# Performance work log

Measured on AMD Instinct MI355X. Metric: run time of the kernel, lower is better.

Reference implementation:

```python
import jax, jax.numpy as jnp
import numpy as np

N, E, H, L, IN, OUT = 50000, 800000, 64, 14, 128, 112
MSG_EPS = 1e-7   # GENConv message epsilon
LN_EPS = 1e-5    # torch.nn.LayerNorm default eps


def setup_inputs() -> dict:
    key = jax.random.key(0)
    ks = jax.random.split(key, 8)
    s = 0.05
    x = jax.random.normal(ks[0], (N, IN), jnp.float32)
    edge_index = jax.random.randint(ks[1], (2, E), 0, N, dtype=jnp.int64)
    enc_W = jax.random.normal(ks[2], (IN, H), jnp.float32) * s
    enc_b = jnp.zeros((H,), jnp.float32)
    ln_g = jnp.ones((L, H), jnp.float32)
    ln_b = jnp.zeros((L, H), jnp.float32)
    mlp_W = jax.random.normal(ks[3], (L, H, H), jnp.float32) * s
    mlp_b = jnp.zeros((L, H), jnp.float32)
    pred_W = jax.random.normal(ks[4], (H, OUT), jnp.float32) * s
    pred_b = jnp.zeros((OUT,), jnp.float32)
    return dict(x=x, edge_index=edge_index, enc_W=enc_W, enc_b=enc_b,
                ln_g=ln_g, ln_b=ln_b, mlp_W=mlp_W, mlp_b=mlp_b,
                pred_W=pred_W, pred_b=pred_b)


def _layernorm(h, g, b):
    mu = jnp.mean(h, axis=-1, keepdims=True)
    var = jnp.mean(jnp.square(h - mu), axis=-1, keepdims=True)  # biased, as torch
    return (h - mu) * jax.lax.rsqrt(var + LN_EPS) * g + b


def _genconv(h, src, dst, W, b):
    # GENConv: msg = relu(x_src) + eps; softmax aggregation (t=1) over dst; out = Linear(x + agg)
    msg = jax.nn.relu(h[src]) + MSG_EPS                    # [E, H]
    mmax = jax.ops.segment_max(msg, dst, num_segments=N)   # [N, H]
    mmax = jnp.where(jnp.isfinite(mmax), mmax, 0.0)         # empty segments
    ex = jnp.exp(msg - mmax[dst])                           # [E, H]
    denom = jax.ops.segment_sum(ex, dst, num_segments=N)    # [N, H]
    num = jax.ops.segment_sum(msg * ex, dst, num_segments=N)
    agg = num / jnp.maximum(denom, 1e-16)                   # 0 for isolated nodes
    return (h + agg) @ W + b


def reference(x, edge_index, enc_W, enc_b, ln_g, ln_b, mlp_W, mlp_b, pred_W, pred_b):
    src, dst = edge_index[0], edge_index[1]
    h = x @ enc_W + enc_b                       # node feature encoder
    h = _genconv(h, src, dst, mlp_W[0], mlp_b[0])  # first GCN (no pre-norm in res+)

    def body(h, params):
        g, bl, W, b = params
        h2 = jax.nn.relu(_layernorm(h, g, bl))  # dropout is identity (eval)
        h = _genconv(h2, src, dst, W, b) + h    # residual
        return h, None

    h, _ = jax.lax.scan(body, h, (ln_g[:L - 1], ln_b[:L - 1], mlp_W[1:], mlp_b[1:]))
    return h @ pred_W + pred_b
```

## Files before the change

### kernel.cpp

```cpp
#include <hip/hip_runtime.h>
#include <hip/hip_bf16.h>

#define NN 50000
#define EE 800000
#define HD 64
#define LL 14
#define IND 128
#define OUTD 112
#define LN2 0.69314718056f

typedef __attribute__((ext_vector_type(8))) short short8;
typedef __attribute__((ext_vector_type(4))) float float4_;
typedef __attribute__((ext_vector_type(4))) unsigned short ushort4_;

__device__ __forceinline__ short bf16_hi(float x) {
    return (short)(__float_as_uint(x) >> 16);
}
__device__ __forceinline__ float bf16_f(short s) {
    return __uint_as_float(((unsigned)(unsigned short)s) << 16);
}
__device__ __forceinline__ float us2f(unsigned short u) {
    return __uint_as_float(((unsigned)u) << 16);
}
__device__ __forceinline__ unsigned short f2b_rne(float x) {
    unsigned u = __float_as_uint(x);
    u += 0x7fffu + ((u >> 16) & 1u);
    return (unsigned short)(u >> 16);
}

__device__ __forceinline__ void split8(const float* p, short8& hi, short8& lo) {
    float4_ a = *(const float4_*)p;
    float4_ b = *(const float4_*)(p + 4);
    float v[8] = {a[0], a[1], a[2], a[3], b[0], b[1], b[2], b[3]};
    #pragma unroll
    for (int j = 0; j < 8; ++j) {
        short h = bf16_hi(v[j]);
        hi[j] = h;
        lo[j] = bf16_hi(v[j] - bf16_f(h));
    }
}

__device__ __forceinline__ void load_b(const float* __restrict__ W, int ldw,
                                       int colbase, int krow, short8& hi, short8& lo) {
    #pragma unroll
    for (int j = 0; j < 8; ++j) {
        float wv = W[(krow + j) * ldw + colbase];
        short h = bf16_hi(wv);
        hi[j] = h;
        lo[j] = bf16_hi(wv - bf16_f(h));
    }
}

__device__ __forceinline__ float4_ mm3(short8 ah, short8 al, short8 bh, short8 bl,
                                       float4_ acc) {
    acc = __builtin_amdgcn_mfma_f32_16x16x32_bf16(ah, bh, acc, 0, 0, 0);
    acc = __builtin_amdgcn_mfma_f32_16x16x32_bf16(al, bh, acc, 0, 0, 0);
    acc = __builtin_amdgcn_mfma_f32_16x16x32_bf16(ah, bl, acc, 0, 0, 0);
    return acc;
}


__global__ void k_hist(const int* __restrict__ ei, int* __restrict__ cnt,
                       int* __restrict__ rank) {
    int e = blockIdx.x * blockDim.x + threadIdx.x;
    if (e < EE) rank[e] = atomicAdd(&cnt[ei[EE + e]], 1);
}

__global__ __launch_bounds__(1024) void k_scan1(const int* __restrict__ deg,
                                                int* __restrict__ excl,
                                                int* __restrict__ bsum) {
    __shared__ int ws[16];
    int tid = threadIdx.x, lane = tid & 63, w = tid >> 6;
    int gid = blockIdx.x * 1024 + tid;
    int v = (gid < NN) ? deg[gid] : 0;
    int x = v;
    #pragma unroll
    for (int d = 1; d < 64; d <<= 1) {
        int y = __shfl_up(x, d);
        if (lane >= d) x += y;
    }
    if (lane == 63) ws[w] = x;
    __syncthreads();
    if (tid == 0) {
        int acc = 0;
        for (int i = 0; i < 16; i++) { int t = ws[i]; ws[i] = acc; acc += t; }
        bsum[blockIdx.x] = acc;
    }
    __syncthreads();
    if (gid < NN) excl[gid] = x - v + ws[w];
}

__global__ void k_scan2(const int* __restrict__ bsum, int* __restrict__ boff, int nb) {
    if (threadIdx.x == 0) {
        int acc = 0;
        for (int i = 0; i < nb; i++) { boff[i] = acc; acc += bsum[i]; }
    }
}

__global__ __launch_bounds__(1024) void k_scan3(int* __restrict__ rp,
                                                const int* __restrict__ boff) {
    int gid = blockIdx.x * 1024 + threadIdx.x;
    if (gid < NN) rp[gid] += boff[blockIdx.x];
    if (gid == 0) rp[NN] = EE;
}

__global__ void k_scatter(const int* __restrict__ ei, const int* __restrict__ rp,
                          const int* __restrict__ rank, int* __restrict__ csrc) {
    int e = blockIdx.x * blockDim.x + threadIdx.x;
    if (e < EE) {
        int d = ei[EE + e];
        csrc[rp[d] + rank[e]] = ei[e];
    }
}


__global__ __launch_bounds__(256) void k_enc(const float* __restrict__ x,
                                             const float* __restrict__ W,
                                             const float* __restrict__ b,
                                             float* __restrict__ h,
                                             unsigned short* __restrict__ P0) {
    __shared__ float X[16 * 132];
    int tid = threadIdx.x, lane = tid & 63, w = tid >> 6;
    int nb = blockIdx.x * 16;
    int nq = lane >> 4, nr = lane & 15;
    int colbase = w * 16 + nr;

    {
        const float* src = x + (size_t)nb * IND + tid * 8;
        float4_ a = *(const float4_*)src;
        float4_ c = *(const float4_*)(src + 4);
        int m = tid >> 4, k8 = 8 * (tid & 15);
        *(float4_*)&X[m * 132 + k8] = a;
        *(float4_*)&X[m * 132 + k8 + 4] = c;
    }
    __syncthreads();

    float4_ acc = {};
    #pragma unroll
    for (int t = 0; t < 4; ++t) {
        short8 ah, al, bh, bl;
        split8(&X[nr * 132 + t * 32 + nq * 8], ah, al);
        load_b(W, HD, colbase, t * 32 + nq * 8, bh, bl);
        acc = mm3(ah, al, bh, bl, acc);
    }

    float bias = b[colbase];
    #pragma unroll
    for (int r = 0; r < 4; ++r) {
        int node = nb + nq * 4 + r;
        float y = acc[r] + bias;
        h[node * HD + colbase] = y;
        float msg = fminf(fmaxf(y, 0.f) + 1e-7f, 50.f);
        P0[node * HD + colbase] = f2b_rne(__expf(msg));
    }
}


__global__ __launch_bounds__(256) void k_layer(const unsigned short* __restrict__ Pin,
                                               const float* __restrict__ selfh,
                                               const float* __restrict__ hres,
                                               float* __restrict__ hout,
                                               unsigned short* __restrict__ Pout,
                                               const int* __restrict__ rp,
                                               const int* __restrict__ csrc,
                                               const float* __restrict__ W,
                                               const float* __restrict__ b,
                                               const float* __restrict__ gnext,
                                               const float* __restrict__ bnext) {
    __shared__ float T[16 * 68];
    int tid = threadIdx.x, lane = tid & 63, w = tid >> 6;
    int nb = blockIdx.x * 16;
    int nq = lane >> 4, nr = lane & 15;
    int colbase = w * 16 + nr;

    short8 Bhi[2], Blo[2];
    #pragma unroll
    for (int t = 0; t < 2; ++t)
        load_b(W, HD, colbase, t * 32 + nq * 8, Bhi[t], Blo[t]);

    int g = lane >> 4;
    int ci = lane & 15;
    #pragma unroll 1
    for (int i = 0; i < 4; ++i) {
        int node = nb + w * 4 + i;
        int beg = rp[node], end = rp[node + 1], deg = end - beg;
        float s0 = 0.f, s1 = 0.f, s2 = 0.f, s3 = 0.f;
        float n0 = 0.f, n1 = 0.f, n2 = 0.f, n3 = 0.f;
        for (int chunk = 0; chunk < deg; chunk += 64) {
            int cnt = min(64, deg - chunk);
            int myidx = 0;
            if (chunk + lane < deg) myidx = csrc[beg + chunk + lane];
            int nb4 = (cnt + 3) >> 2;
            #pragma unroll 2
            for (int k = 0; k < nb4; ++k) {
                int src = __shfl(myidx, k * 4 + g);
                const unsigned* pp = (const unsigned*)(Pin + ((size_t)src << 6)) + ci * 2;
                unsigned d0 = pp[0], d1 = pp[1];
                if (k * 4 + g >= cnt) { d0 = 0u; d1 = 0u; }
                float p0 = __uint_as_float(d0 << 16);
                float p1 = __uint_as_float(d0 & 0xffff0000u);
                float p2 = __uint_as_float(d1 << 16);
                float p3 = __uint_as_float(d1 & 0xffff0000u);
                s0 += p0; s1 += p1; s2 += p2; s3 += p3;
                n0 = fmaf(p0, __log2f(fmaxf(p0, 1e-20f)), n0);
                n1 = fmaf(p1, __log2f(fmaxf(p1, 1e-20f)), n1);
                n2 = fmaf(p2, __log2f(fmaxf(p2, 1e-20f)), n2);
                n3 = fmaf(p3, __log2f(fmaxf(p3, 1e-20f)), n3);
            }
        }
        #pragma unroll
        for (int d = 16; d < 64; d <<= 1) {
            s0 += __shfl_xor(s0, d); s1 += __shfl_xor(s1, d);
            s2 += __shfl_xor(s2, d); s3 += __shfl_xor(s3, d);
            n0 += __shfl_xor(n0, d); n1 += __shfl_xor(n1, d);
            n2 += __shfl_xor(n2, d); n3 += __shfl_xor(n3, d);
        }
        if (g == 0) {
            float a0 = LN2 * n0 / fmaxf(s0, 1e-16f);
            float a1 = LN2 * n1 / fmaxf(s1, 1e-16f);
            float a2 = LN2 * n2 / fmaxf(s2, 1e-16f);
            float a3 = LN2 * n3 / fmaxf(s3, 1e-16f);
            float4_ xv;
            if (selfh) {
                float4_ sf = *(const float4_*)&selfh[(size_t)node * HD + ci * 4];
                xv[0] = sf[0] + a0; xv[1] = sf[1] + a1;
                xv[2] = sf[2] + a2; xv[3] = sf[3] + a3;
            } else {
                const unsigned* pp = (const unsigned*)(Pin + ((size_t)node << 6)) + ci * 2;
                unsigned d0 = pp[0], d1 = pp[1];
                xv[0] = LN2 * __log2f(__uint_as_float(d0 << 16)) - 1e-7f + a0;
                xv[1] = LN2 * __log2f(__uint_as_float(d0 & 0xffff0000u)) - 1e-7f + a1;
                xv[2] = LN2 * __log2f(__uint_as_float(d1 << 16)) - 1e-7f + a2;
                xv[3] = LN2 * __log2f(__uint_as_float(d1 & 0xffff0000u)) - 1e-7f + a3;
            }
            *(float4_*)&T[(w * 4 + i) * 68 + ci * 4] = xv;
        }
    }
    __syncthreads();

    short8 Ahi[2], Alo[2];
    #pragma unroll
    for (int t = 0; t < 2; ++t)
        split8(&T[nr * 68 + t * 32 + nq * 8], Ahi[t], Alo[t]);
    __syncthreads();

    float4_ acc = {};
    #pragma unroll
    for (int t = 0; t < 2; ++t)
        acc = mm3(Ahi[t], Alo[t], Bhi[t], Blo[t], acc);

    float bias = b[colbase];
    #pragma unroll
    for (int r = 0; r < 4; ++r) {
        int m = nq * 4 + r;
        int node = nb + m;
        float v = acc[r] + bias;
        if (hres) v += hres[node * HD + colbase];
        hout[node * HD + colbase] = v;
        T[m * 68 + colbase] = v;
    }
    if (!Pout) return;
    __syncthreads();

    int m = tid >> 4, c4 = (tid & 15) * 4;
    float4_ vv = *(const float4_*)&T[m * 68 + c4];
    float ps_ = (vv[0] + vv[1]) + (vv[2] + vv[3]);
    float pq_ = (vv[0] * vv[0] + vv[1] * vv[1]) + (vv[2] * vv[2] + vv[3] * vv[3]);
    #pragma unroll
    for (int d = 8; d; d >>= 1) {
        ps_ += __shfl_xor(ps_, d);
        pq_ += __shfl_xor(pq_, d);
    }
    float mu = ps_ * (1.f / 64.f);
    float var = pq_ * (1.f / 64.f) - mu * mu;
    float inv = rsqrtf(fmaxf(var, 0.f) + 1e-5f);
    float4_ g4 = *(const float4_*)&gnext[c4];
    float4_ b4 = *(const float4_*)&bnext[c4];
    ushort4_ po;
    #pragma unroll
    for (int j = 0; j < 4; ++j) {
        float y = fmaxf((vv[j] - mu) * inv * g4[j] + b4[j], 0.f);
        float msg = fminf(y + 1e-7f, 50.f);
        po[j] = f2b_rne(__expf(msg));
    }
    *(ushort4_*)&Pout[(nb + m) * HD + c4] = po;
}


__global__ __launch_bounds__(256) void k_pred(const float* __restrict__ h,
                                              const float* __restrict__ W,
                                              const float* __restrict__ b,
                                              float* __restrict__ out) {
    __shared__ float T[16 * 68];
    int tid = threadIdx.x, lane = tid & 63, w = tid >> 6;
    int nb = blockIdx.x * 16;
    int nq = lane >> 4, nr = lane & 15;

    {
        const float* src = h + (size_t)nb * HD + tid * 4;
        float4_ a = *(const float4_*)src;
        int m = tid >> 4, k4 = 4 * (tid & 15);
        *(float4_*)&T[m * 68 + k4] = a;
    }
    __syncthreads();

    short8 Ahi[2], Alo[2];
    #pragma unroll
    for (int t = 0; t < 2; ++t)
        split8(&T[nr * 68 + t * 32 + nq * 8], Ahi[t], Alo[t]);

    for (int tt = w; tt < 7; tt += 4) {
        int colbase = tt * 16 + nr;
        float4_ acc = {};
        #pragma unroll
        for (int t = 0; t < 2; ++t) {
            short8 bh, bl;
            load_b(W, OUTD, colbase, t * 32 + nq * 8, bh, bl);
            acc = mm3(Ahi[t], Alo[t], bh, bl, acc);
        }
        float bias = b[colbase];
        #pragma unroll
        for (int r = 0; r < 4; ++r) {
            int node = nb + nq * 4 + r;
            out[node * OUTD + colbase] = acc[r] + bias;
        }
    }
}


extern "C" void kernel_launch(void* const* d_in, const int* in_sizes, int n_in,
                              void* d_out, int out_size, void* d_ws, size_t ws_size,
                              hipStream_t stream) {
    const float* x    = (const float*)d_in[0];
    const int*   ei   = (const int*)d_in[1];
    const float* encW = (const float*)d_in[2];
    const float* encb = (const float*)d_in[3];
    const float* lng  = (const float*)d_in[4];
    const float* lnb  = (const float*)d_in[5];
    const float* mlpW = (const float*)d_in[6];
    const float* mlpb = (const float*)d_in[7];
    const float* pW   = (const float*)d_in[8];
    const float* pb   = (const float*)d_in[9];
    float* out = (float*)d_out;

    float* hA  = (float*)d_ws;
    float* hB  = hA + (size_t)NN * HD;
    unsigned short* PA = (unsigned short*)(hB + (size_t)NN * HD);
    unsigned short* PB = PA + (size_t)NN * HD;
    int* rp   = (int*)(PB + (size_t)NN * HD);
    int* cnt  = rp + (NN + 1);
    int* csrc = cnt + NN;
    int* rank = csrc + EE;
    int* bsum = rank + EE;
    int* boff = bsum + 64;

    hipMemsetAsync(cnt, 0, NN * sizeof(int), stream);
    k_hist<<<(EE + 255) / 256, 256, 0, stream>>>(ei, cnt, rank);
    const int NB = (NN + 1023) / 1024;
    k_scan1<<<NB, 1024, 0, stream>>>(cnt, rp, bsum);
    k_scan2<<<1, 64, 0, stream>>>(bsum, boff, NB);
    k_scan3<<<NB, 1024, 0, stream>>>(rp, boff);
    k_scatter<<<(EE + 255) / 256, 256, 0, stream>>>(ei, rp, rank, csrc);

    k_enc<<<NN / 16, 256, 0, stream>>>(x, encW, encb, hA, PA);

    k_layer<<<NN / 16, 256, 0, stream>>>(PA, hA, nullptr, hB, PB, rp, csrc,
                                         mlpW, mlpb, lng, lnb);

    float* hres = hB;
    float* hdst = hA;
    unsigned short* pc = PB;
    unsigned short* pn = PA;
    for (int l = 1; l < LL; ++l) {
        bool last = (l == LL - 1);
        k_layer<<<NN / 16, 256, 0, stream>>>(pc, nullptr, hres, hdst,
                                             last ? nullptr : pn,
                                             rp, csrc,
                                             mlpW + (size_t)l * HD * HD,
                                             mlpb + (size_t)l * HD,
                                             last ? nullptr : lng + (size_t)l * HD,
                                             last ? nullptr : lnb + (size_t)l * HD);
        float* t = hres; hres = hdst; hdst = t;
        unsigned short* u = pc; pc = pn; pn = u;
    }

    k_pred<<<NN / 16, 256, 0, stream>>>(hres, pW, pb, out);
}
```

Baseline: 736.2 us.

## Encode exp messages as bf16 codes with shared-memory p·log p lookup table, interleave four nodes

Messages are now stored as small integer codes (bf16 bits of exp(msg) minus an offset), and each block builds a shared-memory table of p and p·ln p for all codes. The per-edge log2 evaluations are replaced by LDS lookups. The four nodes per wave are also gathered in one interleaved loop up to the max degree, so four independent row loads are in flight at once. The cost is a per-block table build of about 1.5K entries with a sync, higher register pressure, and wasted lanes when node degrees differ.

```diff
diff --git a/kernel.cpp b/kernel.cpp
--- a/kernel.cpp
+++ b/kernel.cpp
@@ -8,8 +8,10 @@
 #define IND 128
 #define OUTD 112
 #define LN2 0.69314718056f
+#define LUTN 1537
 
 typedef __attribute__((ext_vector_type(8))) short short8;
+typedef __attribute__((ext_vector_type(2))) float float2_;
 typedef __attribute__((ext_vector_type(4))) float float4_;
 typedef __attribute__((ext_vector_type(4))) unsigned short ushort4_;
 
@@ -18,14 +20,15 @@
 }
 __device__ __forceinline__ float bf16_f(short s) {
     return __uint_as_float(((unsigned)(unsigned short)s) << 16);
-}
-__device__ __forceinline__ float us2f(unsigned short u) {
-    return __uint_as_float(((unsigned)u) << 16);
 }
 __device__ __forceinline__ unsigned short f2b_rne(float x) {
     unsigned u = __float_as_uint(x);
     u += 0x7fffu + ((u >> 16) & 1u);
     return (unsigned short)(u >> 16);
+}
+__device__ __forceinline__ unsigned short msg2code(float msg) {
+    int c = (int)f2b_rne(__expf(msg)) - 16255;
+    return (unsigned short)min(c, 1536);
 }
 
 __device__ __forceinline__ void split8(const float* p, short8& hi, short8& lo) {
@@ -118,7 +121,7 @@
                                              const float* __restrict__ W,
                                              const float* __restrict__ b,
                                              float* __restrict__ h,
-                                             unsigned short* __restrict__ P0) {
+                                             unsigned short* __restrict__ C0) {
     __shared__ float X[16 * 132];
     int tid = threadIdx.x, lane = tid & 63, w = tid >> 6;
     int nb = blockIdx.x * 16;
@@ -151,16 +154,16 @@
         float y = acc[r] + bias;
         h[node * HD + colbase] = y;
         float msg = fminf(fmaxf(y, 0.f) + 1e-7f, 50.f);
-        P0[node * HD + colbase] = f2b_rne(__expf(msg));
-    }
-}
-
-
-__global__ __launch_bounds__(256) void k_layer(const unsigned short* __restrict__ Pin,
+        C0[node * HD + colbase] = msg2code(msg);
+    }
+}
+
+
+__global__ __launch_bounds__(256) void k_layer(const unsigned short* __restrict__ Cin,
                                                const float* __restrict__ selfh,
                                                const float* __restrict__ hres,
                                                float* __restrict__ hout,
-                                               unsigned short* __restrict__ Pout,
+                                               unsigned short* __restrict__ Cout,
                                                const int* __restrict__ rp,
                                                const int* __restrict__ csrc,
                                                const float* __restrict__ W,
@@ -168,46 +171,79 @@
                                                const float* __restrict__ gnext,
                                                const float* __restrict__ bnext) {
     __shared__ float T[16 * 68];
+    __shared__ float L2lut[2 * 1540];
     int tid = threadIdx.x, lane = tid & 63, w = tid >> 6;
     int nb = blockIdx.x * 16;
     int nq = lane >> 4, nr = lane & 15;
     int colbase = w * 16 + nr;
 
+    for (int c = tid; c < LUTN; c += 256) {
+        float p = 0.f, q = 0.f;
+        if (c > 0) {
+            p = __uint_as_float((unsigned)(16255 + c) << 16);
+            q = p * (LN2 * __log2f(p));
+        }
+        L2lut[2 * c] = p;
+        L2lut[2 * c + 1] = q;
+    }
+
     short8 Bhi[2], Blo[2];
     #pragma unroll
     for (int t = 0; t < 2; ++t)
         load_b(W, HD, colbase, t * 32 + nq * 8, Bhi[t], Blo[t]);
+    __syncthreads();
 
     int g = lane >> 4;
     int ci = lane & 15;
-    #pragma unroll 1
+    int node0 = nb + w * 4;
+    int r0 = rp[node0], r1 = rp[node0 + 1], r2 = rp[node0 + 2],
+        r3 = rp[node0 + 3], r4 = rp[node0 + 4];
+    int beg[4] = {r0, r1, r2, r3};
+    int deg[4] = {r1 - r0, r2 - r1, r3 - r2, r4 - r3};
+    int maxdeg = max(max(deg[0], deg[1]), max(deg[2], deg[3]));
+
+    float S[4][4] = {{0.f}}, Nq[4][4] = {{0.f}};
+    for (int chunk = 0; chunk < maxdeg; chunk += 64) {
+        int myidx[4];
+        #pragma unroll
+        for (int i = 0; i < 4; ++i) {
+            myidx[i] = -1;
+            if (chunk + lane < deg[i]) myidx[i] = csrc[beg[i] + chunk + lane];
+        }
+        int cmax = min(64, maxdeg - chunk);
+        int nb4 = (cmax + 3) >> 2;
+        for (int k = 0; k < nb4; ++k) {
+            unsigned d0[4], d1[4];
+            #pragma unroll
+            for (int i = 0; i < 4; ++i) {
+                int src = __shfl(myidx[i], k * 4 + g);
+                const unsigned* pp =
+                    (const unsigned*)(Cin + ((size_t)max(src, 0) << 6)) + ci * 2;
+                unsigned a0 = pp[0], a1 = pp[1];
+                bool act = src >= 0;
+                d0[i] = act ? a0 : 0u;
+                d1[i] = act ? a1 : 0u;
+            }
+            #pragma unroll
+            for (int i = 0; i < 4; ++i) {
+                unsigned c0 = d0[i] & 0xffffu, c1 = d0[i] >> 16;
+                unsigned c2 = d1[i] & 0xffffu, c3 = d1[i] >> 16;
+                float2_ pq0 = *(const float2_*)&L2lut[c0 * 2];
+                float2_ pq1 = *(const float2_*)&L2lut[c1 * 2];
+                float2_ pq2 = *(const float2_*)&L2lut[c2 * 2];
+                float2_ pq3 = *(const float2_*)&L2lut[c3 * 2];
+                S[i][0] += pq0[0]; Nq[i][0] += pq0[1];
+                S[i][1] += pq1[0]; Nq[i][1] += pq1[1];
+                S[i][2] += pq2[0]; Nq[i][2] += pq2[1];
+                S[i][3] += pq3[0]; Nq[i][3] += pq3[1];
+            }
+        }
+    }
+
+    #pragma unroll
     for (int i = 0; i < 4; ++i) {
-        int node = nb + w * 4 + i;
-        int beg = rp[node], end = rp[node + 1], deg = end - beg;
-        float s0 = 0.f, s1 = 0.f, s2 = 0.f, s3 = 0.f;
-        float n0 = 0.f, n1 = 0.f, n2 = 0.f, n3 = 0.f;
-        for (int chunk = 0; chunk < deg; chunk += 64) {
-            int cnt = min(64, deg - chunk);
-            int myidx = 0;
-            if (chunk + lane < deg) myidx = csrc[beg + chunk + lane];
-            int nb4 = (cnt + 3) >> 2;
-            #pragma unroll 2
-            for (int k = 0; k < nb4; ++k) {
-                int src = __shfl(myidx, k * 4 + g);
-                const unsigned* pp = (const unsigned*)(Pin + ((size_t)src << 6)) + ci * 2;
-                unsigned d0 = pp[0], d1 = pp[1];
-                if (k * 4 + g >= cnt) { d0 = 0u; d1 = 0u; }
-                float p0 = __uint_as_float(d0 << 16);
-                float p1 = __uint_as_float(d0 & 0xffff0000u);
-                float p2 = __uint_as_float(d1 << 16);
-                float p3 = __uint_as_float(d1 & 0xffff0000u);
-                s0 += p0; s1 += p1; s2 += p2; s3 += p3;
-                n0 = fmaf(p0, __log2f(fmaxf(p0, 1e-20f)), n0);
-                n1 = fmaf(p1, __log2f(fmaxf(p1, 1e-20f)), n1);
-                n2 = fmaf(p2, __log2f(fmaxf(p2, 1e-20f)), n2);
-                n3 = fmaf(p3, __log2f(fmaxf(p3, 1e-20f)), n3);
-            }
-        }
+        float s0 = S[i][0], s1 = S[i][1], s2 = S[i][2], s3 = S[i][3];
+        float n0 = Nq[i][0], n1 = Nq[i][1], n2 = Nq[i][2], n3 = Nq[i][3];
         #pragma unroll
         for (int d = 16; d < 64; d <<= 1) {
             s0 += __shfl_xor(s0, d); s1 += __shfl_xor(s1, d);
@@ -216,22 +252,27 @@
             n2 += __shfl_xor(n2, d); n3 += __shfl_xor(n3, d);
         }
         if (g == 0) {
-            float a0 = LN2 * n0 / fmaxf(s0, 1e-16f);
-            float a1 = LN2 * n1 / fmaxf(s1, 1e-16f);
-            float a2 = LN2 * n2 / fmaxf(s2, 1e-16f);
-            float a3 = LN2 * n3 / fmaxf(s3, 1e-16f);
+            int node = node0 + i;
+            float a0 = n0 / fmaxf(s0, 1e-16f);
+            float a1 = n1 / fmaxf(s1, 1e-16f);
+            float a2 = n2 / fmaxf(s2, 1e-16f);
+            float a3 = n3 / fmaxf(s3, 1e-16f);
             float4_ xv;
             if (selfh) {
                 float4_ sf = *(const float4_*)&selfh[(size_t)node * HD + ci * 4];
                 xv[0] = sf[0] + a0; xv[1] = sf[1] + a1;
                 xv[2] = sf[2] + a2; xv[3] = sf[3] + a3;
             } else {
-                const unsigned* pp = (const unsigned*)(Pin + ((size_t)node << 6)) + ci * 2;
-                unsigned d0 = pp[0], d1 = pp[1];
-                xv[0] = LN2 * __log2f(__uint_as_float(d0 << 16)) - 1e-7f + a0;
-                xv[1] = LN2 * __log2f(__uint_as_float(d0 & 0xffff0000u)) - 1e-7f + a1;
-                xv[2] = LN2 * __log2f(__uint_as_float(d1 << 16)) - 1e-7f + a2;
-                xv[3] = LN2 * __log2f(__uint_as_float(d1 & 0xffff0000u)) - 1e-7f + a3;
+                const unsigned* pp = (const unsigned*)(Cin + ((size_t)node << 6)) + ci * 2;
+                unsigned e0 = pp[0], e1 = pp[1];
+                float2_ q0 = *(const float2_*)&L2lut[(e0 & 0xffffu) * 2];
+                float2_ q1 = *(const float2_*)&L2lut[(e0 >> 16) * 2];
+                float2_ q2 = *(const float2_*)&L2lut[(e1 & 0xffffu) * 2];
+                float2_ q3 = *(const float2_*)&L2lut[(e1 >> 16) * 2];
+                xv[0] = __fdividef(q0[1], q0[0]) - 1e-7f + a0;
+                xv[1] = __fdividef(q1[1], q1[0]) - 1e-7f + a1;
+                xv[2] = __fdividef(q2[1], q2[0]) - 1e-7f + a2;
+                xv[3] = __fdividef(q3[1], q3[0]) - 1e-7f + a3;
             }
             *(float4_*)&T[(w * 4 + i) * 68 + ci * 4] = xv;
         }
@@ -259,7 +300,7 @@
         hout[node * HD + colbase] = v;
         T[m * 68 + colbase] = v;
     }
-    if (!Pout) return;
+    if (!Cout) return;
     __syncthreads();
 
     int m = tid >> 4, c4 = (tid & 15) * 4;
@@ -281,9 +322,9 @@
     for (int j = 0; j < 4; ++j) {
         float y = fmaxf((vv[j] - mu) * inv * g4[j] + b4[j], 0.f);
         float msg = fminf(y + 1e-7f, 50.f);
-        po[j] = f2b_rne(__expf(msg));
-    }
-    *(ushort4_*)&Pout[(nb + m) * HD + c4] = po;
+        po[j] = msg2code(msg);
+    }
+    *(ushort4_*)&Cout[(nb + m) * HD + c4] = po;
 }
 
 
@@ -345,9 +386,9 @@
 
     float* hA  = (float*)d_ws;
     float* hB  = hA + (size_t)NN * HD;
-    unsigned short* PA = (unsigned short*)(hB + (size_t)NN * HD);
-    unsigned short* PB = PA + (size_t)NN * HD;
-    int* rp   = (int*)(PB + (size_t)NN * HD);
+    unsigned short* CA = (unsigned short*)(hB + (size_t)NN * HD);
+    unsigned short* CB = CA + (size_t)NN * HD;
+    int* rp   = (int*)(CB + (size_t)NN * HD);
     int* cnt  = rp + (NN + 1);
     int* csrc = cnt + NN;
     int* rank = csrc + EE;
@@ -362,26 +403,26 @@
     k_scan3<<<NB, 1024, 0, stream>>>(rp, boff);
     k_scatter<<<(EE + 255) / 256, 256, 0, stream>>>(ei, rp, rank, csrc);
 
-    k_enc<<<NN / 16, 256, 0, stream>>>(x, encW, encb, hA, PA);
-
-    k_layer<<<NN / 16, 256, 0, stream>>>(PA, hA, nullptr, hB, PB, rp, csrc,
+    k_enc<<<NN / 16, 256, 0, stream>>>(x, encW, encb, hA, CA);
+
+    k_layer<<<NN / 16, 256, 0, stream>>>(CA, hA, nullptr, hB, CB, rp, csrc,
                                          mlpW, mlpb, lng, lnb);
 
     float* hres = hB;
     float* hdst = hA;
-    unsigned short* pc = PB;
-    unsigned short* pn = PA;
+    unsigned short* cc = CB;
+    unsigned short* cn = CA;
     for (int l = 1; l < LL; ++l) {
         bool last = (l == LL - 1);
-        k_layer<<<NN / 16, 256, 0, stream>>>(pc, nullptr, hres, hdst,
-                                             last ? nullptr : pn,
+        k_layer<<<NN / 16, 256, 0, stream>>>(cc, nullptr, hres, hdst,
+                                             last ? nullptr : cn,
                                              rp, csrc,
                                              mlpW + (size_t)l * HD * HD,
                                              mlpb + (size_t)l * HD,
                                              last ? nullptr : lng + (size_t)l * HD,
                                              last ? nullptr : lnb + (size_t)l * HD);
         float* t = hres; hres = hdst; hdst = t;
-        unsigned short* u = pc; pc = pn; pn = u;
+        unsigned short* u = cc; cc = cn; cn = u;
     }
 
     k_pred<<<NN / 16, 256, 0, stream>>>(hres, pW, pb, out);
```

Measured after the change: 895.4 us. 21.6% more time.

## Pad CSR rows to multiples of four with a zero sentinel node

Applied to the files above, without the earlier changes.

Each node's CSR row is padded to a multiple of four edges, and the padding slots point to an extra all-zero feature row (index NN) added to both bf16 feature buffers. The aggregation loop then reads edge indices straight from memory per lane group, with no 64-wide chunking, shuffle broadcast or tail masking. This removes per-iteration shuffles and bounds checks from the hot gather loop. In exchange the edge array grows by up to 3N padding entries that each cost a real gather, and two small setup kernels are added. Zero padding rows contribute nothing because p*log2(max(p,eps)) is zero when p is zero.

```diff
diff --git a/kernel.cpp b/kernel.cpp
--- a/kernel.cpp
+++ b/kernel.cpp
@@ -19,9 +19,6 @@
 __device__ __forceinline__ float bf16_f(short s) {
     return __uint_as_float(((unsigned)(unsigned short)s) << 16);
 }
-__device__ __forceinline__ float us2f(unsigned short u) {
-    return __uint_as_float(((unsigned)u) << 16);
-}
 __device__ __forceinline__ unsigned short f2b_rne(float x) {
     unsigned u = __float_as_uint(x);
     u += 0x7fffu + ((u >> 16) & 1u);
@@ -72,7 +69,7 @@
     __shared__ int ws[16];
     int tid = threadIdx.x, lane = tid & 63, w = tid >> 6;
     int gid = blockIdx.x * 1024 + tid;
-    int v = (gid < NN) ? deg[gid] : 0;
+    int v = (gid < NN) ? ((deg[gid] + 3) & ~3) : 0;
     int x = v;
     #pragma unroll
     for (int d = 1; d < 64; d <<= 1) {
@@ -94,14 +91,31 @@
     if (threadIdx.x == 0) {
         int acc = 0;
         for (int i = 0; i < nb; i++) { boff[i] = acc; acc += bsum[i]; }
+        boff[nb] = acc;
     }
 }
 
 __global__ __launch_bounds__(1024) void k_scan3(int* __restrict__ rp,
-                                                const int* __restrict__ boff) {
+                                                const int* __restrict__ boff, int nb) {
     int gid = blockIdx.x * 1024 + threadIdx.x;
     if (gid < NN) rp[gid] += boff[blockIdx.x];
-    if (gid == 0) rp[NN] = EE;
+    if (gid == 0) rp[NN] = boff[nb];
+}
+
+__global__ void k_pad(const int* __restrict__ rp, const int* __restrict__ deg,
+                      int* __restrict__ csrc) {
+    int i = blockIdx.x * blockDim.x + threadIdx.x;
+    if (i < NN) {
+        int base = rp[i], d = deg[i], pd = rp[i + 1] - base;
+        for (int j = d; j < pd; ++j) csrc[base + j] = NN;
+    }
+}
+
+__global__ void k_zrow(unsigned short* __restrict__ PA,
+                       unsigned short* __restrict__ PB) {
+    int t = threadIdx.x;
+    if (t < HD) PA[(size_t)NN * HD + t] = 0;
+    else PB[(size_t)NN * HD + (t - HD)] = 0;
 }
 
 __global__ void k_scatter(const int* __restrict__ ei, const int* __restrict__ rp,
@@ -183,30 +197,25 @@
     #pragma unroll 1
     for (int i = 0; i < 4; ++i) {
         int node = nb + w * 4 + i;
-        int beg = rp[node], end = rp[node + 1], deg = end - beg;
+        int beg = rp[node];
+        int nk = (rp[node + 1] - beg) >> 2;
+        const int* ep = csrc + beg + g;
         float s0 = 0.f, s1 = 0.f, s2 = 0.f, s3 = 0.f;
         float n0 = 0.f, n1 = 0.f, n2 = 0.f, n3 = 0.f;
-        for (int chunk = 0; chunk < deg; chunk += 64) {
-            int cnt = min(64, deg - chunk);
-            int myidx = 0;
-            if (chunk + lane < deg) myidx = csrc[beg + chunk + lane];
-            int nb4 = (cnt + 3) >> 2;
-            #pragma unroll 2
-            for (int k = 0; k < nb4; ++k) {
-                int src = __shfl(myidx, k * 4 + g);
-                const unsigned* pp = (const unsigned*)(Pin + ((size_t)src << 6)) + ci * 2;
-                unsigned d0 = pp[0], d1 = pp[1];
-                if (k * 4 + g >= cnt) { d0 = 0u; d1 = 0u; }
-                float p0 = __uint_as_float(d0 << 16);
-                float p1 = __uint_as_float(d0 & 0xffff0000u);
-                float p2 = __uint_as_float(d1 << 16);
-                float p3 = __uint_as_float(d1 & 0xffff0000u);
-                s0 += p0; s1 += p1; s2 += p2; s3 += p3;
-                n0 = fmaf(p0, __log2f(fmaxf(p0, 1e-20f)), n0);
-                n1 = fmaf(p1, __log2f(fmaxf(p1, 1e-20f)), n1);
-                n2 = fmaf(p2, __log2f(fmaxf(p2, 1e-20f)), n2);
-                n3 = fmaf(p3, __log2f(fmaxf(p3, 1e-20f)), n3);
-            }
+        #pragma unroll 2
+        for (int k = 0; k < nk; ++k) {
+            int src = ep[k * 4];
+            const unsigned* pp = (const unsigned*)(Pin + ((size_t)src << 6)) + ci * 2;
+            unsigned d0 = pp[0], d1 = pp[1];
+            float p0 = __uint_as_float(d0 << 16);
+            float p1 = __uint_as_float(d0 & 0xffff0000u);
+            float p2 = __uint_as_float(d1 << 16);
+            float p3 = __uint_as_float(d1 & 0xffff0000u);
+            s0 += p0; s1 += p1; s2 += p2; s3 += p3;
+            n0 = fmaf(p0, __log2f(fmaxf(p0, 1e-20f)), n0);
+            n1 = fmaf(p1, __log2f(fmaxf(p1, 1e-20f)), n1);
+            n2 = fmaf(p2, __log2f(fmaxf(p2, 1e-20f)), n2);
+            n3 = fmaf(p3, __log2f(fmaxf(p3, 1e-20f)), n3);
         }
         #pragma unroll
         for (int d = 16; d < 64; d <<= 1) {
@@ -346,11 +355,11 @@
     float* hA  = (float*)d_ws;
     float* hB  = hA + (size_t)NN * HD;
     unsigned short* PA = (unsigned short*)(hB + (size_t)NN * HD);
-    unsigned short* PB = PA + (size_t)NN * HD;
-    int* rp   = (int*)(PB + (size_t)NN * HD);
+    unsigned short* PB = PA + (size_t)(NN + 1) * HD;
+    int* rp   = (int*)(PB + (size_t)(NN + 1) * HD);
     int* cnt  = rp + (NN + 1);
     int* csrc = cnt + NN;
-    int* rank = csrc + EE;
+    int* rank = csrc + (EE + 3 * NN + 64);
     int* bsum = rank + EE;
     int* boff = bsum + 64;
 
@@ -359,7 +368,9 @@
     const int NB = (NN + 1023) / 1024;
     k_scan1<<<NB, 1024, 0, stream>>>(cnt, rp, bsum);
     k_scan2<<<1, 64, 0, stream>>>(bsum, boff, NB);
-    k_scan3<<<NB, 1024, 0, stream>>>(rp, boff);
+    k_scan3<<<NB, 1024, 0, stream>>>(rp, boff, NB);
+    k_pad<<<(NN + 255) / 256, 256, 0, stream>>>(rp, cnt, csrc);
+    k_zrow<<<1, 128, 0, stream>>>(PA, PB);
     k_scatter<<<(EE + 255) / 256, 256, 0, stream>>>(ei, rp, rank, csrc);
 
     k_enc<<<NN / 16, 256, 0, stream>>>(x, encW, encb, hA, PA);
```

Measured after the change: 790.2 us. 7.3% more time.
